# Kernel tuning notes

Hardware: AMD Instinct MI355X
Metric: run time of the kernel (lower is better)

## Reference

```python
import jax, jax.numpy as jnp
import numpy as np

D_MODEL = 96
D_INNER = 192   # ssm_ratio * d_model
R = 6           # dt_rank = ceil(96/16)
DH = 32         # d_inner // dt_rank (per-head dim)
K = 4           # scan directions
N = 16          # d_state
EPS = 1e-5


def setup_inputs() -> dict:
    key = jax.random.key(0)
    ks = jax.random.split(key, 10)
    B, H, W = 8, 64, 64
    f = lambda k, s, sc: jax.random.normal(k, s, jnp.float32) * sc
    return dict(
        x=jax.random.normal(ks[0], (B, H, W, D_MODEL), jnp.float32),
        w_in=f(ks[1], (D_MODEL, D_INNER), 0.02),
        w_conv=f(ks[2], (3, 3, 1, D_INNER), 0.1),      # depthwise HWIO
        b_conv=f(ks[3], (D_INNER,), 0.1),
        x_proj_weight=f(ks[4], (K, R + 2 * N, D_INNER), 0.02),
        A_logs=f(ks[5], (K, R), 0.5),
        Ds=jnp.ones((K, R, DH), jnp.float32),
        dt_bias=0.1 * jax.random.uniform(ks[6], (K, R), jnp.float32),
        ln_g=jnp.ones((D_INNER,), jnp.float32),
        ln_b=jnp.zeros((D_INNER,), jnp.float32),
        w_out=f(ks[7], (D_INNER, D_MODEL), 0.02),
    )


def _cross_scan(x):
    # x: (B,H,W,C) -> (B,L,4,C): [row-major, col-major, rev row, rev col]
    B, H, W, C = x.shape
    x0 = x.reshape(B, H * W, C)
    x1 = jnp.transpose(x, (0, 2, 1, 3)).reshape(B, H * W, C)
    return jnp.stack([x0, x1, x0[:, ::-1], x1[:, ::-1]], axis=2)


def _cross_merge(ys, H, W):
    # ys: (B,L,4,C) -> (B,L,C) summed after undoing each scan order
    B, L, _, C = ys.shape
    y_row = ys[:, :, 0] + ys[:, :, 2][:, ::-1]
    y_col = ys[:, :, 1] + ys[:, :, 3][:, ::-1]
    y_col = jnp.transpose(y_col.reshape(B, W, H, C), (0, 2, 1, 3)).reshape(B, L, C)
    return y_row + y_col


def _selective_scan(us, dts, As, Bs, Cs, Dsr, dtb):
    # us:(B,L,KR,DH) dts:(B,L,KR) As:(KR,) Bs,Cs:(B,L,K,N) Dsr:(KR,DH) dtb:(KR,)
    dt = jax.nn.softplus(dts + dtb)                 # (B,L,KR)
    decay = jnp.exp(dt * As)                        # (B,L,KR)
    xu = dt[..., None] * us                         # (B,L,KR,DH)
    Bh = jnp.repeat(Bs, R, axis=2)                  # (B,L,KR,N) head h -> group h//R
    Ch = jnp.repeat(Cs, R, axis=2)
    B_, L, KR, _ = us.shape
    tfirst = lambda a: jnp.moveaxis(a, 1, 0)

    def step(h, inp):
        dec, xu_t, b_t, c_t = inp                   # (B,KR),(B,KR,DH),(B,KR,N),(B,KR,N)
        h = dec[:, :, None, None] * h + xu_t[..., None] * b_t[:, :, None, :]
        y = jnp.einsum('bkdn,bkn->bkd', h, c_t)
        return h, y

    h0 = jnp.zeros((B_, KR, DH, N), us.dtype)
    _, ys = jax.lax.scan(step, h0, (tfirst(decay), tfirst(xu), tfirst(Bh), tfirst(Ch)))
    ys = jnp.moveaxis(ys, 0, 1)                     # (B,L,KR,DH)
    return ys + us * Dsr                            # skip term D*u


def reference(x, w_in, w_conv, b_conv, x_proj_weight, A_logs, Ds, dt_bias, ln_g, ln_b, w_out):
    B, H, W, _ = x.shape
    L = H * W
    xi = x @ w_in                                   # in_proj (no bias)
    xi = jax.lax.conv_general_dilated(
        xi, w_conv, (1, 1), 'SAME', feature_group_count=D_INNER,
        dimension_numbers=('NHWC', 'HWIO', 'NHWC')) + b_conv
    xi = jax.nn.silu(xi)
    xs = _cross_scan(xi)                            # (B,L,4,D_INNER)
    x_dbl = jnp.einsum('blkd,kcd->blkc', xs, x_proj_weight)
    dts = x_dbl[..., :R].reshape(B, L, K * R)
    Bs = x_dbl[..., R:R + N]                        # (B,L,K,N)
    Cs = x_dbl[..., R + N:]
    us = xs.reshape(B, L, K * R, DH)
    As = -jnp.exp(A_logs.astype(jnp.float32)).reshape(K * R)
    Dsr = Ds.reshape(K * R, DH)
    dtb = dt_bias.reshape(K * R)
    ys = _selective_scan(us, dts, As, Bs, Cs, Dsr, dtb)   # (B,L,KR,DH)
    y = _cross_merge(ys.reshape(B, L, K, R * DH), H, W)   # (B,L,D_INNER)
    mu = y.mean(-1, keepdims=True)
    var = ((y - mu) ** 2).mean(-1, keepdims=True)
    y = (y - mu) / jnp.sqrt(var + EPS) * ln_g + ln_b
    y = y.reshape(B, H, W, D_INNER)
    return y @ w_out                                # out_proj (no bias)
```

## Files before the change

kernel.cpp:

```cpp
#include <hip/hip_runtime.h>
#include <hip/hip_bf16.h>

#define BB 8
#define LL 4096
#define DM 96
#define DI 192
#define RRR 6
#define DHH 32
#define KKK 4
#define NNN 16
#define KRR 24
#define NCH 64
#define TT 64
#define RST 48

typedef unsigned short u16;
typedef __attribute__((ext_vector_type(8))) __bf16 bf16x8;
typedef __attribute__((ext_vector_type(4))) float f32x4;

__device__ __forceinline__ float softplus_f(float x){
    float ax = fabsf(x);
    return fmaxf(x, 0.f) + __logf(1.f + __expf(-ax));
}
__device__ __forceinline__ float silu_f(float x){ return x / (1.f + __expf(-x)); }

__device__ __forceinline__ void split_bf16(float v, u16& h, u16& l){
    __bf16 hb = (__bf16)v;
    h = __builtin_bit_cast(u16, hb);
    float r = v - (float)hb;
    l = __builtin_bit_cast(u16, (__bf16)r);
}

__global__ void k0p(const float* __restrict__ W, const float* __restrict__ g,
                    const float* __restrict__ bta, const float* __restrict__ w_out,
                    u16* __restrict__ WhB, u16* __restrict__ WlB,
                    float* __restrict__ wg, float* __restrict__ sgbw){
    int i = blockIdx.x * 256 + threadIdx.x;
    if (i < 2 * 80 * 192){
        int k = i % 192; int n80 = i / 192; int z = n80 / 80; int n = n80 % 80;
        int sub = n / 40, nc = n % 40;
        int dir = (z == 0) ? (sub ? 2 : 0) : (sub ? 3 : 1);
        float v = 0.f;
        if (nc < 6) v = W[(dir * 38 + nc) * DI + k];
        else if (nc >= 8) v = W[(dir * 38 + (nc - 2)) * DI + k];
        u16 h, l; split_bf16(v, h, l);
        WhB[i] = h; WlB[i] = l;
    } else if (i < 30720 + DI * DM){
        int j = i - 30720; int c = j / DM;
        wg[j] = w_out[j] * g[c];
    } else if (i < 30720 + DI * DM + DM){
        int m = i - (30720 + DI * DM);
        float s = 0.f, t = 0.f;
        for (int c = 0; c < DI; ++c){
            float w = w_out[c * DM + m];
            s = fmaf(g[c], w, s);
            t = fmaf(bta[c], w, t);
        }
        sgbw[m] = s; sgbw[DM + m] = t;
    }
}

__global__ __launch_bounds__(384) void k1_inproj(const float* __restrict__ x,
                                                 const float* __restrict__ w_in,
                                                 float* __restrict__ xw){
    __shared__ float xT[DM][36];
    int pix0 = blockIdx.x * 32;
    for (int i = threadIdx.x; i < 32 * 24; i += 384){
        int c4 = i % 24, p = i / 24;
        float4 v = *(const float4*)(x + (size_t)(pix0 + p) * DM + c4 * 4);
        xT[c4 * 4 + 0][p] = v.x; xT[c4 * 4 + 1][p] = v.y;
        xT[c4 * 4 + 2][p] = v.z; xT[c4 * 4 + 3][p] = v.w;
    }
    __syncthreads();
    int cg = threadIdx.x % 48, pg = threadIdx.x / 48;
    int p0 = pg * 4;
    float4 acc[4];
    #pragma unroll
    for (int i = 0; i < 4; ++i) acc[i] = make_float4(0.f, 0.f, 0.f, 0.f);
    const float* wcol = w_in + cg * 4;
    for (int d0 = 0; d0 < DM; d0 += 8){
        float4 wv[8], xv[8];
        #pragma unroll
        for (int j = 0; j < 8; ++j){
            wv[j] = *(const float4*)(wcol + (d0 + j) * DI);
            xv[j] = *(const float4*)(&xT[d0 + j][p0]);
        }
        #pragma unroll
        for (int j = 0; j < 8; ++j){
            float xs[4] = {xv[j].x, xv[j].y, xv[j].z, xv[j].w};
            #pragma unroll
            for (int pi = 0; pi < 4; ++pi){
                acc[pi].x = fmaf(xs[pi], wv[j].x, acc[pi].x);
                acc[pi].y = fmaf(xs[pi], wv[j].y, acc[pi].y);
                acc[pi].z = fmaf(xs[pi], wv[j].z, acc[pi].z);
                acc[pi].w = fmaf(xs[pi], wv[j].w, acc[pi].w);
            }
        }
    }
    #pragma unroll
    for (int pi = 0; pi < 4; ++pi)
        *(float4*)(xw + (size_t)(pix0 + p0 + pi) * DI + cg * 4) = acc[pi];
}

__global__ void k2_conv(const float* __restrict__ xw, const float* __restrict__ wc,
                        const float* __restrict__ bc, float* __restrict__ xi,
                        float* __restrict__ xiT){
    int gid = blockIdx.x * 256 + threadIdx.x;
    int c4 = gid % 48; int pix = gid / 48;
    int b = pix >> 12; int l = pix & 4095; int h = l >> 6; int w = l & 63;
    int c = c4 * 4;
    float4 acc = *(const float4*)(bc + c);
    #pragma unroll
    for (int dh = 0; dh < 3; ++dh){
        int hh = h + dh - 1; if ((unsigned)hh >= 64u) continue;
        #pragma unroll
        for (int dw = 0; dw < 3; ++dw){
            int ww2 = w + dw - 1; if ((unsigned)ww2 >= 64u) continue;
            float4 tap = *(const float4*)(xw + (size_t)((b << 12) + (hh << 6) + ww2) * DI + c);
            float4 wv  = *(const float4*)(wc + (dh * 3 + dw) * DI + c);
            acc.x = fmaf(tap.x, wv.x, acc.x);
            acc.y = fmaf(tap.y, wv.y, acc.y);
            acc.z = fmaf(tap.z, wv.z, acc.z);
            acc.w = fmaf(tap.w, wv.w, acc.w);
        }
    }
    acc.x = silu_f(acc.x); acc.y = silu_f(acc.y); acc.z = silu_f(acc.z); acc.w = silu_f(acc.w);
    *(float4*)(xi + (size_t)pix * DI + c) = acc;
    int lT = ((l & 63) << 6) | (l >> 6);
    *(float4*)(xiT + (size_t)((b << 12) + lT) * DI + c) = acc;
}

__global__ __launch_bounds__(256) void k3seq(const float* __restrict__ xi,
                                             const float* __restrict__ xiT,
                                             const u16* __restrict__ WhB,
                                             const u16* __restrict__ WlB,
                                             const float* __restrict__ A_logs,
                                             const float* __restrict__ dtb,
                                             float* __restrict__ rec){
    __shared__ u16 Xh[64][104];
    __shared__ u16 Xl[64][104];
    int z = blockIdx.y, b = blockIdx.z;
    int l0 = blockIdx.x * 64;
    const float* src = (z ? xiT : xi) + ((((size_t)b) << 12) + l0) * DI;
    int wv = threadIdx.x >> 6, lane = threadIdx.x & 63;
    int quad = lane >> 4, mi = lane & 15;
    int m0 = wv * 16;
    f32x4 acc[5];
    #pragma unroll
    for (int nt = 0; nt < 5; ++nt) acc[nt] = (f32x4){0.f, 0.f, 0.f, 0.f};
    const u16* wh = WhB + (size_t)z * 80 * 192;
    const u16* wl = WlB + (size_t)z * 80 * 192;
    #pragma unroll
    for (int half = 0; half < 2; ++half){
        __syncthreads();
        for (int i = threadIdx.x; i < 1536; i += 256){
            int c4 = i % 24, p = i / 24;
            float4 v = *(const float4*)(src + (size_t)p * DI + half * 96 + c4 * 4);
            u16 h0, h1, h2, h3, q0, q1, q2, q3;
            split_bf16(v.x, h0, q0); split_bf16(v.y, h1, q1);
            split_bf16(v.z, h2, q2); split_bf16(v.w, h3, q3);
            *(ushort4*)&Xh[p][c4 * 4] = make_ushort4(h0, h1, h2, h3);
            *(ushort4*)&Xl[p][c4 * 4] = make_ushort4(q0, q1, q2, q3);
        }
        __syncthreads();
        #pragma unroll
        for (int kt = 0; kt < 3; ++kt){
            int ko = kt * 32 + quad * 8;
            bf16x8 ah = *(const bf16x8*)&Xh[m0 + mi][ko];
            bf16x8 al = *(const bf16x8*)&Xl[m0 + mi][ko];
            int kg = half * 96 + ko;
            #pragma unroll
            for (int nt = 0; nt < 5; ++nt){
                const size_t woff = (size_t)(nt * 16 + mi) * 192 + kg;
                bf16x8 bh = *(const bf16x8*)(wh + woff);
                bf16x8 bl = *(const bf16x8*)(wl + woff);
                acc[nt] = __builtin_amdgcn_mfma_f32_16x16x32_bf16(ah, bh, acc[nt], 0, 0, 0);
                acc[nt] = __builtin_amdgcn_mfma_f32_16x16x32_bf16(al, bh, acc[nt], 0, 0, 0);
                acc[nt] = __builtin_amdgcn_mfma_f32_16x16x32_bf16(ah, bl, acc[nt], 0, 0, 0);
            }
        }
    }
    #pragma unroll
    for (int nt = 0; nt < 5; ++nt){
        int nc = nt * 16 + mi;
        int sub = nc / 40;
        int dir = (z == 0) ? (sub ? 2 : 0) : (sub ? 3 : 1);
        int c40 = nc % 40;
        float* rb = rec + (size_t)(b * KKK + dir) * LL * RST;
        bool isdt = (c40 < 6);
        bool ispad = (c40 == 6) | (c40 == 7);
        float Ac = 0.f, bc = 0.f;
        if (isdt){ Ac = -__expf(A_logs[dir * RRR + c40]); bc = dtb[dir * RRR + c40]; }
        #pragma unroll
        for (int i = 0; i < 4; ++i){
            int l = l0 + m0 + quad * 4 + i;
            int t = (sub == 0) ? l : (LL - 1 - l);
            float v = acc[nt][i];
            float* rw = rb + (size_t)t * RST;
            if (isdt){
                float dt = softplus_f(v + bc);
                rw[c40] = dt;
                rw[c40 + 8] = __expf(dt * Ac);
            } else if (!ispad){
                rw[c40 + 8] = v;
            }
        }
    }
}

__global__ __launch_bounds__(192) void k4a(const float* __restrict__ xi, const float* __restrict__ xiT,
                                           const float* __restrict__ rec,
                                           float* __restrict__ Pb, float* __restrict__ Sb){
    int chunk = blockIdx.x, k = blockIdx.y, b = blockIdx.z;
    int r = threadIdx.x >> 5, d = threadIdx.x & 31;
    int kr = k * RRR + r;
    const float* rp = rec + ((size_t)(b * KKK + k) * LL + chunk * TT) * RST;
    const float* xb = ((k & 1) ? xiT : xi) + (((size_t)b) << 12) * DI + r * DHH + d;
    const float* up; ptrdiff_t ust;
    if (k < 2){ up = xb + (size_t)(chunk * TT) * DI;          ust = DI;  }
    else      { up = xb + (size_t)(LL - 1 - chunk * TT) * DI; ust = -(ptrdiff_t)DI; }
    float h[NNN];
    #pragma unroll
    for (int n = 0; n < NNN; ++n) h[n] = 0.f;
    float P = 1.f;
    #pragma unroll 4
    for (int tt = 0; tt < TT; ++tt){
        float dt  = rp[r];
        float dec = rp[8 + r];
        float u = *up;
        float xu = dt * u;
        P *= dec;
        float Bv[NNN];
        *(float4*)(Bv + 0)  = *(const float4*)(rp + 16);
        *(float4*)(Bv + 4)  = *(const float4*)(rp + 20);
        *(float4*)(Bv + 8)  = *(const float4*)(rp + 24);
        *(float4*)(Bv + 12) = *(const float4*)(rp + 28);
        #pragma unroll
        for (int n = 0; n < NNN; ++n) h[n] = fmaf(dec, h[n], xu * Bv[n]);
        rp += RST; up += ust;
    }
    size_t sb = (((size_t)(b * KRR + kr) * NCH + chunk) * DHH + d) * NNN;
    #pragma unroll
    for (int n = 0; n < NNN; ++n) Sb[sb + n] = h[n];
    if (d == 0) Pb[(size_t)(b * KRR + kr) * NCH + chunk] = P;
}

__global__ __launch_bounds__(256) void k4b(const float* __restrict__ Pb, float* __restrict__ Sb){
    int scan = blockIdx.x >> 1;
    int half = blockIdx.x & 1;
    int tid = half * 256 + threadIdx.x;
    size_t base = (size_t)scan * NCH * 512 + tid;
    const float* Pp = Pb + (size_t)scan * NCH;
    float s[NCH];
    #pragma unroll
    for (int c = 0; c < NCH; ++c) s[c] = Sb[base + (size_t)c * 512];
    float hb = 0.f;
    #pragma unroll
    for (int c = 0; c < NCH; ++c){
        float nv = fmaf(Pp[c], hb, s[c]);
        Sb[base + (size_t)c * 512] = hb;
        hb = nv;
    }
}

__global__ __launch_bounds__(192) void k4c(const float* __restrict__ xi, const float* __restrict__ xiT,
                                           const float* __restrict__ rec,
                                           const float* __restrict__ Ds, const float* __restrict__ Sb,
                                           __hip_bfloat16* __restrict__ ybuf){
    int chunk = blockIdx.x, k = blockIdx.y, b = blockIdx.z;
    int r = threadIdx.x >> 5, d = threadIdx.x & 31;
    int kr = k * RRR + r;
    float Dv = Ds[kr * DHH + d];
    float h[NNN];
    size_t sb = (((size_t)(b * KRR + kr) * NCH + chunk) * DHH + d) * NNN;
    #pragma unroll
    for (int n = 0; n < NNN; ++n) h[n] = Sb[sb + n];
    const float* rp = rec + ((size_t)(b * KKK + k) * LL + chunk * TT) * RST;
    const float* xb = ((k & 1) ? xiT : xi) + (((size_t)b) << 12) * DI + r * DHH + d;
    const float* up; ptrdiff_t ust;
    if (k < 2){ up = xb + (size_t)(chunk * TT) * DI;          ust = DI;  }
    else      { up = xb + (size_t)(LL - 1 - chunk * TT) * DI; ust = -(ptrdiff_t)DI; }
    __hip_bfloat16* yp = ybuf + ((size_t)(k * BB + b) * LL + chunk * TT) * DI + r * DHH + d;
    #pragma unroll 2
    for (int tt = 0; tt < TT; ++tt){
        float dt  = rp[r];
        float dec = rp[8 + r];
        float u = *up;
        float xu = dt * u;
        float Bv[NNN], Cv[NNN];
        *(float4*)(Bv + 0)  = *(const float4*)(rp + 16);
        *(float4*)(Bv + 4)  = *(const float4*)(rp + 20);
        *(float4*)(Bv + 8)  = *(const float4*)(rp + 24);
        *(float4*)(Bv + 12) = *(const float4*)(rp + 28);
        *(float4*)(Cv + 0)  = *(const float4*)(rp + 32);
        *(float4*)(Cv + 4)  = *(const float4*)(rp + 36);
        *(float4*)(Cv + 8)  = *(const float4*)(rp + 40);
        *(float4*)(Cv + 12) = *(const float4*)(rp + 44);
        float y = 0.f;
        #pragma unroll
        for (int n = 0; n < NNN; ++n){
            h[n] = fmaf(dec, h[n], xu * Bv[n]);
            y = fmaf(h[n], Cv[n], y);
        }
        y = fmaf(u, Dv, y);
        *yp = __float2bfloat16(y);
        rp += RST; up += ust; yp += DI;
    }
}

__global__ __launch_bounds__(256) void k5_out(const __hip_bfloat16* __restrict__ ybuf,
                       const float* __restrict__ wg, const float* __restrict__ sgbw,
                       float* __restrict__ out){
    __shared__ float yT[DI][36];
    __shared__ float rsL[32], rmL[32];
    int pix0 = blockIdx.x * 32;
    int b = pix0 >> 12;
    int l0 = pix0 & 4095;
    const __hip_bfloat16* y0 = ybuf + (size_t)(0 * BB + b) * LL * DI;
    const __hip_bfloat16* y1 = ybuf + (size_t)(1 * BB + b) * LL * DI;
    const __hip_bfloat16* y2 = ybuf + (size_t)(2 * BB + b) * LL * DI;
    const __hip_bfloat16* y3 = ybuf + (size_t)(3 * BB + b) * LL * DI;
    for (int i = threadIdx.x; i < 32 * DI; i += 256){
        int c = i % DI, p = i / DI;
        int l = l0 + p; int hh = l >> 6, ww = l & 63;
        int lT = (ww << 6) | hh;
        float s = __bfloat162float(y0[(size_t)l * DI + c])
                + __bfloat162float(y2[(size_t)(LL - 1 - l) * DI + c])
                + __bfloat162float(y1[(size_t)lT * DI + c])
                + __bfloat162float(y3[(size_t)(LL - 1 - lT) * DI + c]);
        yT[c][p] = s;
    }
    __syncthreads();
    {
        int p = threadIdx.x >> 3, cg = threadIdx.x & 7;
        float s = 0.f, s2 = 0.f;
        for (int c = cg; c < DI; c += 8){ float v = yT[c][p]; s += v; s2 = fmaf(v, v, s2); }
        s += __shfl_xor(s, 1, 64); s2 += __shfl_xor(s2, 1, 64);
        s += __shfl_xor(s, 2, 64); s2 += __shfl_xor(s2, 2, 64);
        s += __shfl_xor(s, 4, 64); s2 += __shfl_xor(s2, 4, 64);
        if (cg == 0){
            float mu = s * (1.f / DI);
            float var = s2 * (1.f / DI) - mu * mu;
            float rs = rsqrtf(var + 1e-5f);
            rsL[p] = rs; rmL[p] = rs * mu;
        }
    }
    __syncthreads();
    if (threadIdx.x < 192){
        int mg = threadIdx.x % 24, pg = threadIdx.x / 24;
        int p0 = pg * 4;
        float4 acc[4];
        #pragma unroll
        for (int i = 0; i < 4; ++i) acc[i] = make_float4(0.f, 0.f, 0.f, 0.f);
        const float* wcol = wg + mg * 4;
        for (int c0 = 0; c0 < DI; c0 += 8){
            float4 wv[8], yv[8];
            #pragma unroll
            for (int j = 0; j < 8; ++j){
                wv[j] = *(const float4*)(wcol + (c0 + j) * DM);
                yv[j] = *(const float4*)(&yT[c0 + j][p0]);
            }
            #pragma unroll
            for (int j = 0; j < 8; ++j){
                float ys[4] = {yv[j].x, yv[j].y, yv[j].z, yv[j].w};
                #pragma unroll
                for (int pi = 0; pi < 4; ++pi){
                    acc[pi].x = fmaf(ys[pi], wv[j].x, acc[pi].x);
                    acc[pi].y = fmaf(ys[pi], wv[j].y, acc[pi].y);
                    acc[pi].z = fmaf(ys[pi], wv[j].z, acc[pi].z);
                    acc[pi].w = fmaf(ys[pi], wv[j].w, acc[pi].w);
                }
            }
        }
        float4 sg4 = *(const float4*)(sgbw + mg * 4);
        float4 bw4 = *(const float4*)(sgbw + DM + mg * 4);
        #pragma unroll
        for (int pi = 0; pi < 4; ++pi){
            float rs = rsL[p0 + pi], rm = rmL[p0 + pi];
            float4 o;
            o.x = fmaf(acc[pi].x, rs, fmaf(-rm, sg4.x, bw4.x));
            o.y = fmaf(acc[pi].y, rs, fmaf(-rm, sg4.y, bw4.y));
            o.z = fmaf(acc[pi].z, rs, fmaf(-rm, sg4.z, bw4.z));
            o.w = fmaf(acc[pi].w, rs, fmaf(-rm, sg4.w, bw4.w));
            *(float4*)(out + (size_t)(pix0 + p0 + pi) * DM + mg * 4) = o;
        }
    }
}

extern "C" void kernel_launch(void* const* d_in, const int* in_sizes, int n_in,
                              void* d_out, int out_size, void* d_ws, size_t ws_size,
                              hipStream_t stream){
    const float* x      = (const float*)d_in[0];
    const float* w_in   = (const float*)d_in[1];
    const float* w_conv = (const float*)d_in[2];
    const float* b_conv = (const float*)d_in[3];
    const float* xproj  = (const float*)d_in[4];
    const float* A_logs = (const float*)d_in[5];
    const float* Ds     = (const float*)d_in[6];
    const float* dtbias = (const float*)d_in[7];
    const float* ln_g   = (const float*)d_in[8];
    const float* ln_b   = (const float*)d_in[9];
    const float* w_out  = (const float*)d_in[10];
    float* out = (float*)d_out;

    float* ws   = (float*)d_ws;
    float* xi   = ws;
    float* xiT  = xi + 6291456;
    float* Sb   = xiT + 6291456;
    float* Pb   = Sb + 6291456;
    float* wbase= Pb + 16384;
    u16*   WhB  = (u16*)wbase;
    u16*   WlB  = (u16*)(wbase + 15360);
    float* wg   = wbase + 30720;
    float* sgbw = wg + 18432;
    float* big  = sgbw + 192;
    float* xw   = big;
    float* rec  = big;
    __hip_bfloat16* ybuf = (__hip_bfloat16*)(big + 6291456);

    k0p<<<193, 256, 0, stream>>>(xproj, ln_g, ln_b, w_out, WhB, WlB, wg, sgbw);
    k1_inproj<<<1024, 384, 0, stream>>>(x, w_in, xw);
    k2_conv<<<6144, 256, 0, stream>>>(xw, w_conv, b_conv, xi, xiT);
    k3seq<<<dim3(64, 2, BB), 256, 0, stream>>>(xi, xiT, WhB, WlB, A_logs, dtbias, rec);
    k4a<<<dim3(NCH, KKK, BB), 192, 0, stream>>>(xi, xiT, rec, Pb, Sb);
    k4b<<<384, 256, 0, stream>>>(Pb, Sb);
    k4c<<<dim3(NCH, KKK, BB), 192, 0, stream>>>(xi, xiT, rec, Ds, Sb, ybuf);
    k5_out<<<1024, 256, 0, stream>>>(ybuf, wg, sgbw, out);
}
```

Baseline: 276.7 us.

## Fuse chunked scan into single kernel with decoupled look-back prefix

Replaces the three-kernel chunked selective scan (chunk aggregate, serial prefix over chunks, re-scan with output) with one kernel that publishes per-chunk aggregates and inclusive prefixes through flags, and has each block walk back over predecessor chunks to get its initial state. The chunk length is doubled and the chunk count halved, so fewer state round-trips reach global memory. This removes two launches and the separate prefix pass. It relies on the order in which blocks are scheduled to make forward progress while spinning on flags, and it adds spin-wait latency.

```diff
diff --git a/kernel.cpp b/kernel.cpp
--- a/kernel.cpp
+++ b/kernel.cpp
@@ -10,8 +10,8 @@
 #define KKK 4
 #define NNN 16
 #define KRR 24
-#define NCH 64
-#define TT 64
+#define NC2 32
+#define TT2 128
 #define RST 48
 
 typedef unsigned short u16;
@@ -34,8 +34,10 @@
 __global__ void k0p(const float* __restrict__ W, const float* __restrict__ g,
                     const float* __restrict__ bta, const float* __restrict__ w_out,
                     u16* __restrict__ WhB, u16* __restrict__ WlB,
-                    float* __restrict__ wg, float* __restrict__ sgbw){
+                    float* __restrict__ wg, float* __restrict__ sgbw,
+                    int* __restrict__ flags){
     int i = blockIdx.x * 256 + threadIdx.x;
+    if (i < 192 * NC2) flags[i] = 0;
     if (i < 2 * 80 * 192){
         int k = i % 192; int n80 = i / 192; int z = n80 / 80; int n = n80 % 80;
         int sub = n / 40, nc = n % 40;
@@ -208,103 +210,126 @@
     }
 }
 
-__global__ __launch_bounds__(192) void k4a(const float* __restrict__ xi, const float* __restrict__ xiT,
-                                           const float* __restrict__ rec,
-                                           float* __restrict__ Pb, float* __restrict__ Sb){
+__global__ __launch_bounds__(192, 4) void k4scan(const float* __restrict__ xi,
+                                                 const float* __restrict__ xiT,
+                                                 const float* __restrict__ rec,
+                                                 const float* __restrict__ Ds,
+                                                 float* __restrict__ Sagg,
+                                                 float* __restrict__ Sinc,
+                                                 float* __restrict__ Pb,
+                                                 int* __restrict__ flags,
+                                                 __hip_bfloat16* __restrict__ ybuf){
     int chunk = blockIdx.x, k = blockIdx.y, b = blockIdx.z;
     int r = threadIdx.x >> 5, d = threadIdx.x & 31;
     int kr = k * RRR + r;
-    const float* rp = rec + ((size_t)(b * KKK + k) * LL + chunk * TT) * RST;
+    int scan = (b * KKK + k) * RRR + r;
+    const float* rp0 = rec + ((size_t)(b * KKK + k) * LL + chunk * TT2) * RST;
     const float* xb = ((k & 1) ? xiT : xi) + (((size_t)b) << 12) * DI + r * DHH + d;
-    const float* up; ptrdiff_t ust;
-    if (k < 2){ up = xb + (size_t)(chunk * TT) * DI;          ust = DI;  }
-    else      { up = xb + (size_t)(LL - 1 - chunk * TT) * DI; ust = -(ptrdiff_t)DI; }
+    const float* up0; ptrdiff_t ust;
+    if (k < 2){ up0 = xb + (size_t)(chunk * TT2) * DI;          ust = DI;  }
+    else      { up0 = xb + (size_t)(LL - 1 - chunk * TT2) * DI; ust = -(ptrdiff_t)DI; }
+
     float h[NNN];
     #pragma unroll
     for (int n = 0; n < NNN; ++n) h[n] = 0.f;
     float P = 1.f;
-    #pragma unroll 4
-    for (int tt = 0; tt < TT; ++tt){
-        float dt  = rp[r];
-        float dec = rp[8 + r];
-        float u = *up;
-        float xu = dt * u;
-        P *= dec;
-        float Bv[NNN];
-        *(float4*)(Bv + 0)  = *(const float4*)(rp + 16);
-        *(float4*)(Bv + 4)  = *(const float4*)(rp + 20);
-        *(float4*)(Bv + 8)  = *(const float4*)(rp + 24);
-        *(float4*)(Bv + 12) = *(const float4*)(rp + 28);
-        #pragma unroll
-        for (int n = 0; n < NNN; ++n) h[n] = fmaf(dec, h[n], xu * Bv[n]);
-        rp += RST; up += ust;
-    }
-    size_t sb = (((size_t)(b * KRR + kr) * NCH + chunk) * DHH + d) * NNN;
-    #pragma unroll
-    for (int n = 0; n < NNN; ++n) Sb[sb + n] = h[n];
-    if (d == 0) Pb[(size_t)(b * KRR + kr) * NCH + chunk] = P;
-}
-
-__global__ __launch_bounds__(256) void k4b(const float* __restrict__ Pb, float* __restrict__ Sb){
-    int scan = blockIdx.x >> 1;
-    int half = blockIdx.x & 1;
-    int tid = half * 256 + threadIdx.x;
-    size_t base = (size_t)scan * NCH * 512 + tid;
-    const float* Pp = Pb + (size_t)scan * NCH;
-    float s[NCH];
-    #pragma unroll
-    for (int c = 0; c < NCH; ++c) s[c] = Sb[base + (size_t)c * 512];
-    float hb = 0.f;
-    #pragma unroll
-    for (int c = 0; c < NCH; ++c){
-        float nv = fmaf(Pp[c], hb, s[c]);
-        Sb[base + (size_t)c * 512] = hb;
-        hb = nv;
-    }
-}
-
-__global__ __launch_bounds__(192) void k4c(const float* __restrict__ xi, const float* __restrict__ xiT,
-                                           const float* __restrict__ rec,
-                                           const float* __restrict__ Ds, const float* __restrict__ Sb,
-                                           __hip_bfloat16* __restrict__ ybuf){
-    int chunk = blockIdx.x, k = blockIdx.y, b = blockIdx.z;
-    int r = threadIdx.x >> 5, d = threadIdx.x & 31;
-    int kr = k * RRR + r;
+    {
+        const float* rp = rp0; const float* up = up0;
+        #pragma unroll 4
+        for (int tt = 0; tt < TT2; ++tt){
+            float dt  = rp[r];
+            float dec = rp[8 + r];
+            float u = *up;
+            float xu = dt * u;
+            P *= dec;
+            float Bv[NNN];
+            *(float4*)(Bv + 0)  = *(const float4*)(rp + 16);
+            *(float4*)(Bv + 4)  = *(const float4*)(rp + 20);
+            *(float4*)(Bv + 8)  = *(const float4*)(rp + 24);
+            *(float4*)(Bv + 12) = *(const float4*)(rp + 28);
+            #pragma unroll
+            for (int n = 0; n < NNN; ++n) h[n] = fmaf(dec, h[n], xu * Bv[n]);
+            rp += RST; up += ust;
+        }
+    }
+    size_t sb = (((size_t)scan * NC2 + chunk) << 9) + d * 16;
+    if (d == 0) Pb[scan * NC2 + chunk] = P;
+    #pragma unroll
+    for (int n = 0; n < NNN; n += 4) *(float4*)(Sagg + sb + n) = *(float4*)(h + n);
+    __threadfence();
+    if (d == 0)
+        __hip_atomic_store(flags + scan * NC2 + chunk, 1, __ATOMIC_RELEASE, __HIP_MEMORY_SCOPE_AGENT);
+
+    float hi[NNN];
+    #pragma unroll
+    for (int n = 0; n < NNN; ++n) hi[n] = 0.f;
+    if (chunk > 0){
+        float prefP = 1.f;
+        int j = chunk - 1;
+        while (true){
+            int fl;
+            while ((fl = __hip_atomic_load(flags + scan * NC2 + j, __ATOMIC_ACQUIRE,
+                                           __HIP_MEMORY_SCOPE_AGENT)) == 0)
+                __builtin_amdgcn_s_sleep(1);
+            const float* Sp = ((fl == 2) ? Sinc : Sagg) + (((size_t)scan * NC2 + j) << 9) + d * 16;
+            float Sv[NNN];
+            *(float4*)(Sv + 0)  = *(const float4*)(Sp + 0);
+            *(float4*)(Sv + 4)  = *(const float4*)(Sp + 4);
+            *(float4*)(Sv + 8)  = *(const float4*)(Sp + 8);
+            *(float4*)(Sv + 12) = *(const float4*)(Sp + 12);
+            #pragma unroll
+            for (int n = 0; n < NNN; ++n) hi[n] = fmaf(prefP, Sv[n], hi[n]);
+            if (fl == 2 || j == 0) break;
+            prefP *= Pb[scan * NC2 + j];
+            --j;
+        }
+    }
+    if (chunk > 0 && chunk < NC2 - 1){
+        #pragma unroll
+        for (int n = 0; n < NNN; n += 4){
+            float4 v;
+            v.x = fmaf(P, hi[n + 0], h[n + 0]);
+            v.y = fmaf(P, hi[n + 1], h[n + 1]);
+            v.z = fmaf(P, hi[n + 2], h[n + 2]);
+            v.w = fmaf(P, hi[n + 3], h[n + 3]);
+            *(float4*)(Sinc + sb + n) = v;
+        }
+        __threadfence();
+        if (d == 0)
+            __hip_atomic_store(flags + scan * NC2 + chunk, 2, __ATOMIC_RELEASE, __HIP_MEMORY_SCOPE_AGENT);
+    }
+
     float Dv = Ds[kr * DHH + d];
-    float h[NNN];
-    size_t sb = (((size_t)(b * KRR + kr) * NCH + chunk) * DHH + d) * NNN;
-    #pragma unroll
-    for (int n = 0; n < NNN; ++n) h[n] = Sb[sb + n];
-    const float* rp = rec + ((size_t)(b * KKK + k) * LL + chunk * TT) * RST;
-    const float* xb = ((k & 1) ? xiT : xi) + (((size_t)b) << 12) * DI + r * DHH + d;
-    const float* up; ptrdiff_t ust;
-    if (k < 2){ up = xb + (size_t)(chunk * TT) * DI;          ust = DI;  }
-    else      { up = xb + (size_t)(LL - 1 - chunk * TT) * DI; ust = -(ptrdiff_t)DI; }
-    __hip_bfloat16* yp = ybuf + ((size_t)(k * BB + b) * LL + chunk * TT) * DI + r * DHH + d;
-    #pragma unroll 2
-    for (int tt = 0; tt < TT; ++tt){
-        float dt  = rp[r];
-        float dec = rp[8 + r];
-        float u = *up;
-        float xu = dt * u;
-        float Bv[NNN], Cv[NNN];
-        *(float4*)(Bv + 0)  = *(const float4*)(rp + 16);
-        *(float4*)(Bv + 4)  = *(const float4*)(rp + 20);
-        *(float4*)(Bv + 8)  = *(const float4*)(rp + 24);
-        *(float4*)(Bv + 12) = *(const float4*)(rp + 28);
-        *(float4*)(Cv + 0)  = *(const float4*)(rp + 32);
-        *(float4*)(Cv + 4)  = *(const float4*)(rp + 36);
-        *(float4*)(Cv + 8)  = *(const float4*)(rp + 40);
-        *(float4*)(Cv + 12) = *(const float4*)(rp + 44);
-        float y = 0.f;
-        #pragma unroll
-        for (int n = 0; n < NNN; ++n){
-            h[n] = fmaf(dec, h[n], xu * Bv[n]);
-            y = fmaf(h[n], Cv[n], y);
-        }
-        y = fmaf(u, Dv, y);
-        *yp = __float2bfloat16(y);
-        rp += RST; up += ust; yp += DI;
+    #pragma unroll
+    for (int n = 0; n < NNN; ++n) h[n] = hi[n];
+    {
+        const float* rp = rp0; const float* up = up0;
+        __hip_bfloat16* yp = ybuf + ((size_t)(k * BB + b) * LL + chunk * TT2) * DI + r * DHH + d;
+        #pragma unroll 2
+        for (int tt = 0; tt < TT2; ++tt){
+            float dt  = rp[r];
+            float dec = rp[8 + r];
+            float u = *up;
+            float xu = dt * u;
+            float Bv[NNN], Cv[NNN];
+            *(float4*)(Bv + 0)  = *(const float4*)(rp + 16);
+            *(float4*)(Bv + 4)  = *(const float4*)(rp + 20);
+            *(float4*)(Bv + 8)  = *(const float4*)(rp + 24);
+            *(float4*)(Bv + 12) = *(const float4*)(rp + 28);
+            *(float4*)(Cv + 0)  = *(const float4*)(rp + 32);
+            *(float4*)(Cv + 4)  = *(const float4*)(rp + 36);
+            *(float4*)(Cv + 8)  = *(const float4*)(rp + 40);
+            *(float4*)(Cv + 12) = *(const float4*)(rp + 44);
+            float y = 0.f;
+            #pragma unroll
+            for (int n = 0; n < NNN; ++n){
+                h[n] = fmaf(dec, h[n], xu * Bv[n]);
+                y = fmaf(h[n], Cv[n], y);
+            }
+            y = fmaf(u, Dv, y);
+            *yp = __float2bfloat16(y);
+            rp += RST; up += ust; yp += DI;
+        }
     }
 }
 
@@ -406,9 +431,11 @@
     float* ws   = (float*)d_ws;
     float* xi   = ws;
     float* xiT  = xi + 6291456;
-    float* Sb   = xiT + 6291456;
-    float* Pb   = Sb + 6291456;
-    float* wbase= Pb + 16384;
+    float* Sagg = xiT + 6291456;
+    float* Sinc = Sagg + 3145728;
+    float* Pb   = Sinc + 3145728;
+    int*   flags= (int*)(Pb + 6144);
+    float* wbase= Pb + 6144 + 6144;
     u16*   WhB  = (u16*)wbase;
     u16*   WlB  = (u16*)(wbase + 15360);
     float* wg   = wbase + 30720;
@@ -418,12 +445,10 @@
     float* rec  = big;
     __hip_bfloat16* ybuf = (__hip_bfloat16*)(big + 6291456);
 
-    k0p<<<193, 256, 0, stream>>>(xproj, ln_g, ln_b, w_out, WhB, WlB, wg, sgbw);
+    k0p<<<193, 256, 0, stream>>>(xproj, ln_g, ln_b, w_out, WhB, WlB, wg, sgbw, flags);
     k1_inproj<<<1024, 384, 0, stream>>>(x, w_in, xw);
     k2_conv<<<6144, 256, 0, stream>>>(xw, w_conv, b_conv, xi, xiT);
     k3seq<<<dim3(64, 2, BB), 256, 0, stream>>>(xi, xiT, WhB, WlB, A_logs, dtbias, rec);
-    k4a<<<dim3(NCH, KKK, BB), 192, 0, stream>>>(xi, xiT, rec, Pb, Sb);
-    k4b<<<384, 256, 0, stream>>>(Pb, Sb);
-    k4c<<<dim3(NCH, KKK, BB), 192, 0, stream>>>(xi, xiT, rec, Ds, Sb, ybuf);
+    k4scan<<<dim3(NC2, KKK, BB), 192, 0, stream>>>(xi, xiT, rec, Ds, Sagg, Sinc, Pb, flags, ybuf);
     k5_out<<<1024, 256, 0, stream>>>(ybuf, wg, sgbw, out);
 }
```

Result: slower. 847.1 us (+206.1%).

## Fuse chunk-local scan with output and add cheap carry-in correction pass

Applied to the files above, without the earlier changes.

The first chunked-scan pass now computes the zero-initialised local state and the chunk-local output y together, storing the cumulative decay product per timestep. After the inter-chunk carry pass, a light correction kernel adds C·h_in·cumprod to the stored bf16 outputs instead of rerunning the full recurrence with B loads and state updates. This removes one full sequential scan over x and B, at the cost of an extra bf16 read-modify-write of ybuf (a second rounding) and a new per-timestep decay-product buffer.

```diff
diff --git a/kernel.cpp b/kernel.cpp
--- a/kernel.cpp
+++ b/kernel.cpp
@@ -209,84 +209,31 @@
 }
 
 __global__ __launch_bounds__(192) void k4a(const float* __restrict__ xi, const float* __restrict__ xiT,
-                                           const float* __restrict__ rec,
-                                           float* __restrict__ Pb, float* __restrict__ Sb){
-    int chunk = blockIdx.x, k = blockIdx.y, b = blockIdx.z;
-    int r = threadIdx.x >> 5, d = threadIdx.x & 31;
-    int kr = k * RRR + r;
-    const float* rp = rec + ((size_t)(b * KKK + k) * LL + chunk * TT) * RST;
-    const float* xb = ((k & 1) ? xiT : xi) + (((size_t)b) << 12) * DI + r * DHH + d;
-    const float* up; ptrdiff_t ust;
-    if (k < 2){ up = xb + (size_t)(chunk * TT) * DI;          ust = DI;  }
-    else      { up = xb + (size_t)(LL - 1 - chunk * TT) * DI; ust = -(ptrdiff_t)DI; }
-    float h[NNN];
-    #pragma unroll
-    for (int n = 0; n < NNN; ++n) h[n] = 0.f;
-    float P = 1.f;
-    #pragma unroll 4
-    for (int tt = 0; tt < TT; ++tt){
-        float dt  = rp[r];
-        float dec = rp[8 + r];
-        float u = *up;
-        float xu = dt * u;
-        P *= dec;
-        float Bv[NNN];
-        *(float4*)(Bv + 0)  = *(const float4*)(rp + 16);
-        *(float4*)(Bv + 4)  = *(const float4*)(rp + 20);
-        *(float4*)(Bv + 8)  = *(const float4*)(rp + 24);
-        *(float4*)(Bv + 12) = *(const float4*)(rp + 28);
-        #pragma unroll
-        for (int n = 0; n < NNN; ++n) h[n] = fmaf(dec, h[n], xu * Bv[n]);
-        rp += RST; up += ust;
-    }
-    size_t sb = (((size_t)(b * KRR + kr) * NCH + chunk) * DHH + d) * NNN;
-    #pragma unroll
-    for (int n = 0; n < NNN; ++n) Sb[sb + n] = h[n];
-    if (d == 0) Pb[(size_t)(b * KRR + kr) * NCH + chunk] = P;
-}
-
-__global__ __launch_bounds__(256) void k4b(const float* __restrict__ Pb, float* __restrict__ Sb){
-    int scan = blockIdx.x >> 1;
-    int half = blockIdx.x & 1;
-    int tid = half * 256 + threadIdx.x;
-    size_t base = (size_t)scan * NCH * 512 + tid;
-    const float* Pp = Pb + (size_t)scan * NCH;
-    float s[NCH];
-    #pragma unroll
-    for (int c = 0; c < NCH; ++c) s[c] = Sb[base + (size_t)c * 512];
-    float hb = 0.f;
-    #pragma unroll
-    for (int c = 0; c < NCH; ++c){
-        float nv = fmaf(Pp[c], hb, s[c]);
-        Sb[base + (size_t)c * 512] = hb;
-        hb = nv;
-    }
-}
-
-__global__ __launch_bounds__(192) void k4c(const float* __restrict__ xi, const float* __restrict__ xiT,
-                                           const float* __restrict__ rec,
-                                           const float* __restrict__ Ds, const float* __restrict__ Sb,
-                                           __hip_bfloat16* __restrict__ ybuf){
+                                           const float* __restrict__ rec, const float* __restrict__ Ds,
+                                           float* __restrict__ Pb, float* __restrict__ Sb,
+                                           float* __restrict__ pp, __hip_bfloat16* __restrict__ ybuf){
     int chunk = blockIdx.x, k = blockIdx.y, b = blockIdx.z;
     int r = threadIdx.x >> 5, d = threadIdx.x & 31;
     int kr = k * RRR + r;
     float Dv = Ds[kr * DHH + d];
-    float h[NNN];
-    size_t sb = (((size_t)(b * KRR + kr) * NCH + chunk) * DHH + d) * NNN;
-    #pragma unroll
-    for (int n = 0; n < NNN; ++n) h[n] = Sb[sb + n];
     const float* rp = rec + ((size_t)(b * KKK + k) * LL + chunk * TT) * RST;
     const float* xb = ((k & 1) ? xiT : xi) + (((size_t)b) << 12) * DI + r * DHH + d;
     const float* up; ptrdiff_t ust;
     if (k < 2){ up = xb + (size_t)(chunk * TT) * DI;          ust = DI;  }
     else      { up = xb + (size_t)(LL - 1 - chunk * TT) * DI; ust = -(ptrdiff_t)DI; }
     __hip_bfloat16* yp = ybuf + ((size_t)(k * BB + b) * LL + chunk * TT) * DI + r * DHH + d;
+    float* ppp = pp + ((size_t)(b * KKK + k) * RRR + r) * LL + chunk * TT;
+    float h[NNN];
+    #pragma unroll
+    for (int n = 0; n < NNN; ++n) h[n] = 0.f;
+    float ppv = 1.f;
     #pragma unroll 2
     for (int tt = 0; tt < TT; ++tt){
         float dt  = rp[r];
         float dec = rp[8 + r];
         float u = *up;
         float xu = dt * u;
+        ppv *= dec;
         float Bv[NNN], Cv[NNN];
         *(float4*)(Bv + 0)  = *(const float4*)(rp + 16);
         *(float4*)(Bv + 4)  = *(const float4*)(rp + 20);
@@ -304,7 +251,62 @@
         }
         y = fmaf(u, Dv, y);
         *yp = __float2bfloat16(y);
+        if (d == 0) ppp[tt] = ppv;
         rp += RST; up += ust; yp += DI;
+    }
+    size_t sb = (((size_t)(b * KRR + kr) * NCH + chunk) * DHH + d) * NNN;
+    #pragma unroll
+    for (int n = 0; n < NNN; ++n) Sb[sb + n] = h[n];
+    if (d == 0) Pb[(size_t)(b * KRR + kr) * NCH + chunk] = ppv;
+}
+
+__global__ __launch_bounds__(256) void k4b(const float* __restrict__ Pb, float* __restrict__ Sb){
+    int scan = blockIdx.x >> 1;
+    int half = blockIdx.x & 1;
+    int tid = half * 256 + threadIdx.x;
+    size_t base = (size_t)scan * NCH * 512 + tid;
+    const float* Pp = Pb + (size_t)scan * NCH;
+    float s[NCH];
+    #pragma unroll
+    for (int c = 0; c < NCH; ++c) s[c] = Sb[base + (size_t)c * 512];
+    float hb = 0.f;
+    #pragma unroll
+    for (int c = 0; c < NCH; ++c){
+        float nv = fmaf(Pp[c], hb, s[c]);
+        Sb[base + (size_t)c * 512] = hb;
+        hb = nv;
+    }
+}
+
+__global__ __launch_bounds__(192) void k4corr(const float* __restrict__ rec,
+                                              const float* __restrict__ Sb,
+                                              const float* __restrict__ pp,
+                                              __hip_bfloat16* __restrict__ ybuf){
+    int chunk = blockIdx.x + 1;
+    int k = blockIdx.y, b = blockIdx.z;
+    int r = threadIdx.x >> 5, d = threadIdx.x & 31;
+    int kr = k * RRR + r;
+    float hi[NNN];
+    size_t sb = (((size_t)(b * KRR + kr) * NCH + chunk) * DHH + d) * NNN;
+    #pragma unroll
+    for (int n = 0; n < NNN; ++n) hi[n] = Sb[sb + n];
+    const float* rp = rec + ((size_t)(b * KKK + k) * LL + chunk * TT) * RST + 32;
+    const float* ppp = pp + ((size_t)(b * KKK + k) * RRR + r) * LL + chunk * TT;
+    __hip_bfloat16* yp = ybuf + ((size_t)(k * BB + b) * LL + chunk * TT) * DI + r * DHH + d;
+    #pragma unroll 4
+    for (int tt = 0; tt < TT; ++tt){
+        float Cv[NNN];
+        *(float4*)(Cv + 0)  = *(const float4*)(rp + 0);
+        *(float4*)(Cv + 4)  = *(const float4*)(rp + 4);
+        *(float4*)(Cv + 8)  = *(const float4*)(rp + 8);
+        *(float4*)(Cv + 12) = *(const float4*)(rp + 12);
+        float dv = 0.f;
+        #pragma unroll
+        for (int n = 0; n < NNN; ++n) dv = fmaf(hi[n], Cv[n], dv);
+        float y = __bfloat162float(*yp);
+        y = fmaf(ppp[tt], dv, y);
+        *yp = __float2bfloat16(y);
+        rp += RST; yp += DI;
     }
 }
 
@@ -408,7 +410,8 @@
     float* xiT  = xi + 6291456;
     float* Sb   = xiT + 6291456;
     float* Pb   = Sb + 6291456;
-    float* wbase= Pb + 16384;
+    float* pp   = Pb + 16384;
+    float* wbase= pp + 786432;
     u16*   WhB  = (u16*)wbase;
     u16*   WlB  = (u16*)(wbase + 15360);
     float* wg   = wbase + 30720;
@@ -422,8 +425,8 @@
     k1_inproj<<<1024, 384, 0, stream>>>(x, w_in, xw);
     k2_conv<<<6144, 256, 0, stream>>>(xw, w_conv, b_conv, xi, xiT);
     k3seq<<<dim3(64, 2, BB), 256, 0, stream>>>(xi, xiT, WhB, WlB, A_logs, dtbias, rec);
-    k4a<<<dim3(NCH, KKK, BB), 192, 0, stream>>>(xi, xiT, rec, Pb, Sb);
+    k4a<<<dim3(NCH, KKK, BB), 192, 0, stream>>>(xi, xiT, rec, Ds, Pb, Sb, pp, ybuf);
     k4b<<<384, 256, 0, stream>>>(Pb, Sb);
-    k4c<<<dim3(NCH, KKK, BB), 192, 0, stream>>>(xi, xiT, rec, Ds, Sb, ybuf);
+    k4corr<<<dim3(NCH - 1, KKK, BB), 192, 0, stream>>>(rec, Sb, pp, ybuf);
     k5_out<<<1024, 256, 0, stream>>>(ybuf, wg, sgbw, out);
 }
```

New measurement: 279.4 us. No clear change (+1.0%).
